# Kernel optimization log

Hardware: AMD Instinct MI355X
Metric: run time of the kernel (lower is better)

The kernel has to match this reference:

```python
import jax, jax.numpy as jnp
import numpy as np

SEQ_LEN = 512
DIM = 256
HEADS = 8
DIM_HEAD = 32
INNER = HEADS * DIM_HEAD
BATCH = 1
LN_EPS = 1e-5


def setup_inputs() -> dict:
    key = jax.random.key(0)
    ks = jax.random.split(key, 6)
    # kaiming_uniform_(a=sqrt(5)) on [L, in, out] -> bound = 1/sqrt(fan_in) with fan_in = in_dim*out_dim? 
    # torch computes fan_in from dims [1:] => fan_in = in_dim (dim of -2) * ... in practice bound ~ sqrt(1/fan_in);
    # exact init distribution is irrelevant for correctness testing, use uniform(+-1/sqrt(DIM)).
    s = 1.0 / np.sqrt(DIM)
    so = 1.0 / np.sqrt(INNER)
    return {
        "x": jax.random.normal(ks[0], (BATCH, SEQ_LEN, DIM), jnp.float32),
        "Wq": jax.random.uniform(ks[1], (SEQ_LEN, DIM, INNER), jnp.float32, -s, s),
        "Wk": jax.random.uniform(ks[2], (SEQ_LEN, DIM, INNER), jnp.float32, -s, s),
        "Wv": jax.random.uniform(ks[3], (SEQ_LEN, DIM, INNER), jnp.float32, -s, s),
        "gamma": jnp.ones((DIM,), jnp.float32),
        "beta": jnp.zeros((DIM,), jnp.float32),
        "Wo": jax.random.uniform(ks[4], (INNER, DIM), jnp.float32, -so, so),
        "bo": jnp.zeros((DIM,), jnp.float32),
    }


def reference(x, Wq, Wk, Wv, gamma, beta, Wo, bo):
    b, n, dim = x.shape
    h, dh = HEADS, DIM_HEAD
    # LayerNorm
    mu = jnp.mean(x, axis=-1, keepdims=True)
    var = jnp.mean((x - mu) ** 2, axis=-1, keepdims=True)
    xn = (x - mu) / jnp.sqrt(var + LN_EPS) * gamma + beta
    # Per-relative-index projections: pd[b, r, m, e] = xn[b, m] @ W[r]
    qd = jnp.einsum('bmc,rce->brme', xn, Wq)
    kd = jnp.einsum('bmc,rce->brme', xn, Wk)
    vd = jnp.einsum('bmc,rce->brme', xn, Wv)
    i = jnp.arange(n)
    # to_q / to_v index map: max(0, i - j); to_k (after rearrange swap) uses min(0, m - n) + n - 1
    rq = jnp.maximum(0, i[:, None] - i[None, :])          # [n(query), m(key)]
    rk = jnp.minimum(0, i[None, :] - i[:, None]) + n - 1  # [n, m]
    # q[b,n,m,e] = qd[b, rq[n,m], m]; k[b,n,m,e] = kd[b, rk[n,m], n]; v like q
    q_full = qd[:, rq, i[None, :], :].reshape(b, n, n, h, dh)
    k_full = kd[:, rk, i[:, None], :].reshape(b, n, n, h, dh)
    v_full = vd[:, rq, i[None, :], :].reshape(b, n, n, h, dh)
    scale = dh ** -0.5
    dots = jnp.einsum('bnmhd,bnmhd->bhnm', q_full, k_full) * scale
    causal = i[:, None] >= i[None, :]  # tril
    dots = jnp.where(causal[None, None], dots, -jnp.inf)
    attn = jax.nn.softmax(dots, axis=-1)
    out = jnp.einsum('bhnm,bnmhd->bnhd', attn, v_full).reshape(b, n, h * dh)
    return out @ Wo + bo
```

## Files before the change

kernel.cpp:

```cpp
#include <hip/hip_runtime.h>
#include <hip/hip_bf16.h>

typedef unsigned short u16;
typedef unsigned int   u32;
typedef __bf16 bf16x8 __attribute__((ext_vector_type(8)));
typedef float  f32x4  __attribute__((ext_vector_type(4)));
typedef u32    u32x4  __attribute__((ext_vector_type(4)));
typedef u32    u32x2  __attribute__((ext_vector_type(2)));

#define TRI_TOTAL 131328

__device__ __forceinline__ float b2f(u16 u) {
    return __builtin_bit_cast(float, ((u32)u) << 16);
}
__device__ __forceinline__ u16 f2b(float f) {
    return __builtin_bit_cast(u16, __float2bfloat16(f));
}
__device__ __forceinline__ int pcol(int col) {
    return (((col & 7) ^ ((col >> 3) & 7)) << 4);
}
__device__ __forceinline__ void gload_lds16(const void* g, void* l) {
    __builtin_amdgcn_global_load_lds(
        (const __attribute__((address_space(1))) void*)g,
        (__attribute__((address_space(3))) void*)l, 16, 0, 0);
}

__global__ void __launch_bounds__(256) ln_kernel(const float* __restrict__ x,
                                                 const float* __restrict__ g,
                                                 const float* __restrict__ b,
                                                 u16* __restrict__ xn) {
    int n = blockIdx.x, t = threadIdx.x;
    float v = x[n * 256 + t];
    __shared__ float red[4];
    float s = v;
    #pragma unroll
    for (int o = 32; o >= 1; o >>= 1) s += __shfl_xor(s, o);
    if ((t & 63) == 0) red[t >> 6] = s;
    __syncthreads();
    float mu = (red[0] + red[1] + red[2] + red[3]) * (1.0f / 256.0f);
    float d = v - mu;
    __syncthreads();
    float s2 = d * d;
    #pragma unroll
    for (int o = 32; o >= 1; o >>= 1) s2 += __shfl_xor(s2, o);
    if ((t & 63) == 0) red[t >> 6] = s2;
    __syncthreads();
    float var = (red[0] + red[1] + red[2] + red[3]) * (1.0f / 256.0f);
    float y = d * rsqrtf(var + 1e-5f) * g[t] + b[t];
    xn[n * 256 + t] = f2b(y);
}

__global__ void __launch_bounds__(256) proj_kernel(
        const u16* __restrict__ xn,
        const float* __restrict__ Wq, const float* __restrict__ Wk,
        const float* __restrict__ Wv,
        u16* __restrict__ Qa, u16* __restrict__ Ka, u16* __restrict__ Va) {
    __shared__ char lds[65536];
    char* buf0 = lds;
    char* buf1 = lds + 32768;

    int bid = blockIdx.x;
    int which = bid >> 11;
    int rr = bid & 2047;
    int r  = (which == 1) ? (511 - (rr >> 2)) : (rr >> 2);
    int cs = rr & 3;
    const float* W = (which == 0) ? Wq : ((which == 1) ? Wk : Wv);
    u16* Out       = (which == 0) ? Qa : ((which == 1) ? Ka : Va);
    int rows  = (which == 1) ? (r + 1) : (512 - r);
    int pbase = (which == 1) ? (511 - r) : 0;
    int nbase = (which == 1) ? (511 - r) : r;

    int t = threadIdx.x;
    int c0 = cs * 64;
    int wv  = t >> 6;
    int rg  = wv >> 1;
    int cg  = wv & 1;
    int L   = t & 63;
    int l15 = L & 15, l4 = L >> 4;

#define DMA_TILE(DST, M0) do {                                                \
    _Pragma("unroll")                                                         \
    for (int j = 0; j < 8; ++j) {                                             \
        int lrow = wv * 16 + 2 * j + (L >> 5);                                \
        int grow = pbase + (M0) + lrow; if (grow > 511) grow = 511;           \
        const char* gp = (const char*)xn + (size_t)grow * 512                 \
                         + (((L & 31) ^ (lrow & 7)) << 4);                    \
        char* lp = (DST) + (wv * 16 + 2 * j) * 512;                           \
        gload_lds16(gp, lp);                                                  \
    }                                                                         \
} while (0)

    DMA_TILE(buf1, 0);

    {
        int c4 = (t & 15) * 4;
        int kq = t >> 4;
        const float* wp = W + ((size_t)r << 16) + c0 + c4 + (size_t)(kq * 4) * 256;
        f32x4 w00 = *(const f32x4*)(wp + 0);
        f32x4 w01 = *(const f32x4*)(wp + 256);
        f32x4 w02 = *(const f32x4*)(wp + 512);
        f32x4 w03 = *(const f32x4*)(wp + 768);
        f32x4 w10 = *(const f32x4*)(wp + 16384 + 0);
        f32x4 w11 = *(const f32x4*)(wp + 16384 + 256);
        f32x4 w12 = *(const f32x4*)(wp + 16384 + 512);
        f32x4 w13 = *(const f32x4*)(wp + 16384 + 768);
        f32x4 w20 = *(const f32x4*)(wp + 32768 + 0);
        f32x4 w21 = *(const f32x4*)(wp + 32768 + 256);
        f32x4 w22 = *(const f32x4*)(wp + 32768 + 512);
        f32x4 w23 = *(const f32x4*)(wp + 32768 + 768);
        f32x4 w30 = *(const f32x4*)(wp + 49152 + 0);
        f32x4 w31 = *(const f32x4*)(wp + 49152 + 256);
        f32x4 w32 = *(const f32x4*)(wp + 49152 + 512);
        f32x4 w33 = *(const f32x4*)(wp + 49152 + 768);
#define WLW(IT, VA, VB, VC, VD) {                                             \
        int kbase2 = (kq * 4 + (IT) * 64) * 2;                                \
        _Pragma("unroll")                                                     \
        for (int i = 0; i < 4; ++i) {                                         \
            int col = c4 + i;                                                 \
            u32 lo = (u32)f2b(VA[i]) | ((u32)f2b(VB[i]) << 16);               \
            u32 hi = (u32)f2b(VC[i]) | ((u32)f2b(VD[i]) << 16);               \
            u32x2 pr; pr[0] = lo; pr[1] = hi;                                 \
            *(u32x2*)(buf0 + col * 512 + (kbase2 ^ pcol(col))) = pr;          \
        }                                                                     \
    }
        WLW(0, w00, w01, w02, w03)
        WLW(1, w10, w11, w12, w13)
        WLW(2, w20, w21, w22, w23)
        WLW(3, w30, w31, w32, w33)
#undef WLW
    }
    __syncthreads();

    bf16x8 b00, b01, b02, b03, b04, b05, b06, b07;
    bf16x8 b10, b11, b12, b13, b14, b15, b16, b17;
#define BEXT(HF, KSI, DST) {                                                  \
    int col = cg * 32 + (HF) * 16 + l15;                                      \
    int kb = (KSI) * 64 + l4 * 16;                                            \
    DST = *(const bf16x8*)(buf0 + col * 512 + (kb ^ pcol(col))); }
    BEXT(0, 0, b00) BEXT(0, 1, b01) BEXT(0, 2, b02) BEXT(0, 3, b03)
    BEXT(0, 4, b04) BEXT(0, 5, b05) BEXT(0, 6, b06) BEXT(0, 7, b07)
    BEXT(1, 0, b10) BEXT(1, 1, b11) BEXT(1, 2, b12) BEXT(1, 3, b13)
    BEXT(1, 4, b14) BEXT(1, 5, b15) BEXT(1, 6, b16) BEXT(1, 7, b17)
#undef BEXT
    __syncthreads();

    int am = (l15 & 7) << 4;
    int nt = (rows + 63) >> 6;
    char* cur = buf1;
    char* alt = buf0;

    for (int i = 0; i < nt; ++i) {
        int m0 = i << 6;
        if (i + 1 < nt) DMA_TILE(alt, m0 + 64);

        const char* abase = cur + (rg * 32 + l15) * 512;
        f32x4 acc00 = {}, acc01 = {}, acc10 = {}, acc11 = {};
#define KS(ks) {                                                              \
        int kb = (ks) * 64 + l4 * 16;                                         \
        bf16x8 a0 = *(const bf16x8*)(abase + (kb ^ am));                      \
        bf16x8 a1 = *(const bf16x8*)(abase + 16 * 512 + (kb ^ am));           \
        acc00 = __builtin_amdgcn_mfma_f32_16x16x32_bf16(a0, b0##ks, acc00, 0, 0, 0); \
        acc01 = __builtin_amdgcn_mfma_f32_16x16x32_bf16(a0, b1##ks, acc01, 0, 0, 0); \
        acc10 = __builtin_amdgcn_mfma_f32_16x16x32_bf16(a1, b0##ks, acc10, 0, 0, 0); \
        acc11 = __builtin_amdgcn_mfma_f32_16x16x32_bf16(a1, b1##ks, acc11, 0, 0, 0); \
    }
        KS(0) KS(1) KS(2) KS(3) KS(4) KS(5) KS(6) KS(7)
#undef KS

        #pragma unroll
        for (int rf = 0; rf < 2; ++rf) {
            #pragma unroll
            for (int j = 0; j < 4; ++j) {
                int ml = m0 + rg * 32 + rf * 16 + l4 * 4 + j;
                if (ml < rows) {
                    u32 nout = (u32)(nbase + ml);
                    u32 prow = (nout * (nout + 1)) >> 1;
                    u16* op = Out + (size_t)((u32)(prow + (u32)ml)) * 256
                              + c0 + cg * 32 + l15;
                    f32x4 va = rf ? acc10 : acc00;
                    f32x4 vb = rf ? acc11 : acc01;
                    op[0]  = f2b(va[j]);
                    op[16] = f2b(vb[j]);
                }
            }
        }
        asm volatile("s_waitcnt vmcnt(16)" ::: "memory");
        __builtin_amdgcn_s_barrier();
        __builtin_amdgcn_sched_barrier(0);
        char* tmp = cur; cur = alt; alt = tmp;
    }
#undef DMA_TILE
}

__global__ void __launch_bounds__(256) attn_kernel(const u16* __restrict__ Qa,
                                                   const u16* __restrict__ Ka,
                                                   const u16* __restrict__ Va,
                                                   float* __restrict__ ao) {
    int n = blockIdx.x, t = threadIdx.x;
    __shared__ float pbuf[512 * 9];
    __shared__ float linv[8];
    int band = n + 1;
    size_t rb = (size_t)(n * (n + 1) / 2);

    int h = t & 7, mi = t >> 3;
    for (int m0 = 0; m0 < band; m0 += 32) {
        int m = m0 + mi;
        float d = -1e30f;
        if (m < band) {
            const char* qp = (const char*)Qa + (rb + m) * 512 + h * 64;
            const char* kp = (const char*)Ka + (rb + m) * 512 + h * 64;
            float acc = 0.f;
            #pragma unroll
            for (int cch = 0; cch < 4; ++cch) {
                u32x4 qv = *reinterpret_cast<const u32x4*>(qp + cch * 16);
                u32x4 kv = *reinterpret_cast<const u32x4*>(kp + cch * 16);
                #pragma unroll
                for (int i = 0; i < 4; ++i) {
                    float ql = __builtin_bit_cast(float, qv[i] << 16);
                    float qh = __builtin_bit_cast(float, qv[i] & 0xffff0000u);
                    float kl = __builtin_bit_cast(float, kv[i] << 16);
                    float kh = __builtin_bit_cast(float, kv[i] & 0xffff0000u);
                    acc += ql * kl + qh * kh;
                }
            }
            d = acc * 0.17677669529663687f;
        }
        pbuf[m * 9 + h] = d;
    }
    __syncthreads();

    int wv = t >> 6, L = t & 63;
    for (int s = 0; s < 2; ++s) {
        int hh = wv + s * 4;
        float mx = -1e30f;
        for (int m = L; m < band; m += 64) mx = fmaxf(mx, pbuf[m * 9 + hh]);
        #pragma unroll
        for (int o = 32; o >= 1; o >>= 1) mx = fmaxf(mx, __shfl_xor(mx, o));
        float sum = 0.f;
        for (int m = L; m < band; m += 64) {
            float p = __expf(pbuf[m * 9 + hh] - mx);
            pbuf[m * 9 + hh] = p;
            sum += p;
        }
        #pragma unroll
        for (int o = 32; o >= 1; o >>= 1) sum += __shfl_xor(sum, o);
        if (L == 0) linv[hh] = 1.0f / sum;
    }
    __syncthreads();

    int h2 = t >> 5;
    const char* vp = (const char*)Va + rb * 512 + (size_t)t * 2;
    const float* pb = pbuf + h2;
    float a0 = 0, a1 = 0, a2 = 0, a3 = 0;
    int m = 0;
    for (; m + 4 <= band; m += 4) {
        a0 += pb[(m + 0) * 9] * b2f(*(const u16*)(vp + (size_t)(m + 0) * 512));
        a1 += pb[(m + 1) * 9] * b2f(*(const u16*)(vp + (size_t)(m + 1) * 512));
        a2 += pb[(m + 2) * 9] * b2f(*(const u16*)(vp + (size_t)(m + 2) * 512));
        a3 += pb[(m + 3) * 9] * b2f(*(const u16*)(vp + (size_t)(m + 3) * 512));
    }
    for (; m < band; ++m)
        a0 += pb[m * 9] * b2f(*(const u16*)(vp + (size_t)m * 512));
    ao[n * 256 + t] = ((a0 + a1) + (a2 + a3)) * linv[h2];
}

__global__ void __launch_bounds__(256) outproj_kernel(const float* __restrict__ ao,
                                                      const float* __restrict__ Wo,
                                                      const float* __restrict__ bo,
                                                      float* __restrict__ out) {
    int n = blockIdx.x, e = threadIdx.x;
    const float* a = ao + n * 256;
    float c0 = bo[e], c1 = 0, c2 = 0, c3 = 0;
    for (int c = 0; c < 256; c += 4) {
        c0 += a[c + 0] * Wo[(c + 0) * 256 + e];
        c1 += a[c + 1] * Wo[(c + 1) * 256 + e];
        c2 += a[c + 2] * Wo[(c + 2) * 256 + e];
        c3 += a[c + 3] * Wo[(c + 3) * 256 + e];
    }
    out[n * 256 + e] = (c0 + c1) + (c2 + c3);
}

extern "C" void kernel_launch(void* const* d_in, const int* in_sizes, int n_in,
                              void* d_out, int out_size, void* d_ws, size_t ws_size,
                              hipStream_t stream) {
    const float* x     = (const float*)d_in[0];
    const float* Wq    = (const float*)d_in[1];
    const float* Wk    = (const float*)d_in[2];
    const float* Wv    = (const float*)d_in[3];
    const float* gamma = (const float*)d_in[4];
    const float* beta  = (const float*)d_in[5];
    const float* Wo    = (const float*)d_in[6];
    const float* bo    = (const float*)d_in[7];
    float* out = (float*)d_out;

    char* ws = (char*)d_ws;
    u16* xn = (u16*)ws;
    size_t off = (size_t)512 * 256 * 2;
    u16* Qa = (u16*)(ws + off); off += (size_t)TRI_TOTAL * 256 * 2;
    u16* Ka = (u16*)(ws + off); off += (size_t)TRI_TOTAL * 256 * 2;
    u16* Va = (u16*)(ws + off); off += (size_t)TRI_TOTAL * 256 * 2;
    float* ao = (float*)(ws + off);

    ln_kernel<<<512, 256, 0, stream>>>(x, gamma, beta, xn);
    proj_kernel<<<6144, 256, 0, stream>>>(xn, Wq, Wk, Wv, Qa, Ka, Va);
    attn_kernel<<<512, 256, 0, stream>>>(Qa, Ka, Va, ao);
    outproj_kernel<<<512, 256, 0, stream>>>(ao, Wo, bo, out);
}
```

Measured before the change: 263.3 us.

## Load projection A operand directly from global instead of double-buffered LDS DMA

Removes the double-buffered global-to-LDS DMA pipeline for the normalized input tiles in the projection kernel. MFMA A operands are now read straight from global memory (xn is small and likely L2-resident), and the per-tile barriers and wait counts go away. LDS use drops from 64KB to 32KB, which could raise occupancy. The cost is that the loads are no longer prefetched, so global load latency is exposed inside the MFMA loop.

```diff
diff --git a/kernel.cpp b/kernel.cpp
--- a/kernel.cpp
+++ b/kernel.cpp
@@ -18,11 +18,6 @@
 }
 __device__ __forceinline__ int pcol(int col) {
     return (((col & 7) ^ ((col >> 3) & 7)) << 4);
-}
-__device__ __forceinline__ void gload_lds16(const void* g, void* l) {
-    __builtin_amdgcn_global_load_lds(
-        (const __attribute__((address_space(1))) void*)g,
-        (__attribute__((address_space(3))) void*)l, 16, 0, 0);
 }
 
 __global__ void __launch_bounds__(256) ln_kernel(const float* __restrict__ x,
@@ -55,9 +50,7 @@
         const float* __restrict__ Wq, const float* __restrict__ Wk,
         const float* __restrict__ Wv,
         u16* __restrict__ Qa, u16* __restrict__ Ka, u16* __restrict__ Va) {
-    __shared__ char lds[65536];
-    char* buf0 = lds;
-    char* buf1 = lds + 32768;
+    __shared__ u16 Wl[64 * 256];
 
     int bid = blockIdx.x;
     int which = bid >> 11;
@@ -77,20 +70,6 @@
     int cg  = wv & 1;
     int L   = t & 63;
     int l15 = L & 15, l4 = L >> 4;
-
-#define DMA_TILE(DST, M0) do {                                                \
-    _Pragma("unroll")                                                         \
-    for (int j = 0; j < 8; ++j) {                                             \
-        int lrow = wv * 16 + 2 * j + (L >> 5);                                \
-        int grow = pbase + (M0) + lrow; if (grow > 511) grow = 511;           \
-        const char* gp = (const char*)xn + (size_t)grow * 512                 \
-                         + (((L & 31) ^ (lrow & 7)) << 4);                    \
-        char* lp = (DST) + (wv * 16 + 2 * j) * 512;                           \
-        gload_lds16(gp, lp);                                                  \
-    }                                                                         \
-} while (0)
-
-    DMA_TILE(buf1, 0);
 
     {
         int c4 = (t & 15) * 4;
@@ -120,7 +99,7 @@
             u32 lo = (u32)f2b(VA[i]) | ((u32)f2b(VB[i]) << 16);               \
             u32 hi = (u32)f2b(VC[i]) | ((u32)f2b(VD[i]) << 16);               \
             u32x2 pr; pr[0] = lo; pr[1] = hi;                                 \
-            *(u32x2*)(buf0 + col * 512 + (kbase2 ^ pcol(col))) = pr;          \
+            *(u32x2*)((char*)Wl + col * 512 + (kbase2 ^ pcol(col))) = pr;     \
         }                                                                     \
     }
         WLW(0, w00, w01, w02, w03)
@@ -136,29 +115,24 @@
 #define BEXT(HF, KSI, DST) {                                                  \
     int col = cg * 32 + (HF) * 16 + l15;                                      \
     int kb = (KSI) * 64 + l4 * 16;                                            \
-    DST = *(const bf16x8*)(buf0 + col * 512 + (kb ^ pcol(col))); }
+    DST = *(const bf16x8*)((const char*)Wl + col * 512 + (kb ^ pcol(col))); }
     BEXT(0, 0, b00) BEXT(0, 1, b01) BEXT(0, 2, b02) BEXT(0, 3, b03)
     BEXT(0, 4, b04) BEXT(0, 5, b05) BEXT(0, 6, b06) BEXT(0, 7, b07)
     BEXT(1, 0, b10) BEXT(1, 1, b11) BEXT(1, 2, b12) BEXT(1, 3, b13)
     BEXT(1, 4, b14) BEXT(1, 5, b15) BEXT(1, 6, b16) BEXT(1, 7, b17)
 #undef BEXT
-    __syncthreads();
-
-    int am = (l15 & 7) << 4;
-    int nt = (rows + 63) >> 6;
-    char* cur = buf1;
-    char* alt = buf0;
-
-    for (int i = 0; i < nt; ++i) {
-        int m0 = i << 6;
-        if (i + 1 < nt) DMA_TILE(alt, m0 + 64);
-
-        const char* abase = cur + (rg * 32 + l15) * 512;
+
+    for (int m0 = 0; m0 < rows; m0 += 64) {
+        int mlo = m0 + rg * 32 + l15;
+        int g0 = pbase + mlo;       if (g0 > 511) g0 = 511;
+        int g1 = pbase + mlo + 16;  if (g1 > 511) g1 = 511;
+        const char* s0 = (const char*)xn + (size_t)g0 * 512 + l4 * 16;
+        const char* s1 = (const char*)xn + (size_t)g1 * 512 + l4 * 16;
+
         f32x4 acc00 = {}, acc01 = {}, acc10 = {}, acc11 = {};
 #define KS(ks) {                                                              \
-        int kb = (ks) * 64 + l4 * 16;                                         \
-        bf16x8 a0 = *(const bf16x8*)(abase + (kb ^ am));                      \
-        bf16x8 a1 = *(const bf16x8*)(abase + 16 * 512 + (kb ^ am));           \
+        bf16x8 a0 = *(const bf16x8*)(s0 + (ks) * 64);                         \
+        bf16x8 a1 = *(const bf16x8*)(s1 + (ks) * 64);                         \
         acc00 = __builtin_amdgcn_mfma_f32_16x16x32_bf16(a0, b0##ks, acc00, 0, 0, 0); \
         acc01 = __builtin_amdgcn_mfma_f32_16x16x32_bf16(a0, b1##ks, acc01, 0, 0, 0); \
         acc10 = __builtin_amdgcn_mfma_f32_16x16x32_bf16(a1, b0##ks, acc10, 0, 0, 0); \
@@ -175,7 +149,7 @@
                 if (ml < rows) {
                     u32 nout = (u32)(nbase + ml);
                     u32 prow = (nout * (nout + 1)) >> 1;
-                    u16* op = Out + (size_t)((u32)(prow + (u32)ml)) * 256
+                    u16* op = Out + (size_t)(prow + (u32)ml) * 256
                               + c0 + cg * 32 + l15;
                     f32x4 va = rf ? acc10 : acc00;
                     f32x4 vb = rf ? acc11 : acc01;
@@ -184,12 +158,7 @@
                 }
             }
         }
-        asm volatile("s_waitcnt vmcnt(16)" ::: "memory");
-        __builtin_amdgcn_s_barrier();
-        __builtin_amdgcn_sched_barrier(0);
-        char* tmp = cur; cur = alt; alt = tmp;
-    }
-#undef DMA_TILE
+    }
 }
 
 __global__ void __launch_bounds__(256) attn_kernel(const u16* __restrict__ Qa,
```

Result: slower. 354.6 us (+34.7%).
